# Kernel tuning notes

Measured on AMD Instinct MI355X. Metric: run time of the kernel, lower is better.

The kernel has to match this reference:

```python
import jax, jax.numpy as jnp
import numpy as np

M_DIM = 128   # vec_dim m
L_BAS = 64    # bas_dim L
RANK = 8      # sliding window length
BATCH = 32
SEQ = 2048


def _make_bbasis(L, m):
    # Bbasis[k, i] = cos(2*pi*(k+1)/(i+2)), fixed buffer
    k = jnp.arange(L, dtype=jnp.float32)[:, None]
    i = jnp.arange(m, dtype=jnp.float32)[None, :]
    return jnp.cos(2.0 * jnp.pi * (k + 1.0) / (i + 2.0))


def setup_inputs() -> dict:
    key = jax.random.key(0)
    k1, k2 = jax.random.split(key)
    seq_batch = jax.random.normal(k1, (BATCH, SEQ, M_DIM), dtype=jnp.float32)
    M = jnp.eye(M_DIM, dtype=jnp.float32)                     # nn.init.eye_
    Acoeff = jax.random.uniform(k2, (M_DIM, L_BAS), dtype=jnp.float32,
                                minval=-0.1, maxval=0.1)      # uniform(-0.1, 0.1)
    Bbasis = _make_bbasis(L_BAS, M_DIM)
    return {"seq_batch": seq_batch, "M": M, "Acoeff": Acoeff, "Bbasis": Bbasis}


def reference(seq_batch, M, Acoeff, Bbasis):
    B, S, m = seq_batch.shape
    L = Acoeff.shape[1]
    Nw = S - RANK + 1  # number of sliding windows (linear mode, stride 1)

    # unfold-equivalent: gather contiguous windows [B, Nw, RANK, m]
    idx = jnp.arange(Nw)[:, None] + jnp.arange(RANK)[None, :]
    windows = seq_batch[:, idx, :]
    agg = windows.mean(axis=2)              # rank_op='avg' -> [B, Nw, m]
    agg = jnp.einsum('bwm,nm->bwn', agg, M)  # agg @ M.T (linear map)

    # position-indexed basis target: N(k)[i] = Acoeff[i, k%L] * Bbasis[k%L, i]
    kmod = jnp.arange(Nw) % L
    Nk = Acoeff.T[kmod] * Bbasis[kmod]       # [Nw, m]

    # mean squared deviation over all windows / dims
    D = jnp.mean((agg - Nk[None, :, :]) ** 2)
    return D
```

## Files before the change

kernel.cpp:

```cpp
#include <hip/hip_runtime.h>

#define BATCH   32
#define SEQ     2048
#define MDIM    128
#define LBAS    64
#define NW      2041
#define TW      16
#define NTILE   8
#define APAD    136

typedef __attribute__((ext_vector_type(8))) short  short8;
typedef __attribute__((ext_vector_type(4))) float  float4v;

__device__ __forceinline__ unsigned short f2bf(float f) {
    unsigned int u = __float_as_uint(f);
    return (unsigned short)((u + 0x7FFFu + ((u >> 16) & 1u)) >> 16);
}
__device__ __forceinline__ void store_bf16x4(unsigned short* p, float4v a) {
    unsigned int lo = (unsigned)f2bf(a.x) | ((unsigned)f2bf(a.y) << 16);
    unsigned int hi = (unsigned)f2bf(a.z) | ((unsigned)f2bf(a.w) << 16);
    *reinterpret_cast<unsigned long long*>(p) = ((unsigned long long)hi << 32) | lo;
}

__global__ __launch_bounds__(256)
void ndd_prep(const float* __restrict__ Mmat,
              const float* __restrict__ Acoeff,
              const float* __restrict__ Bbasis,
              unsigned short* __restrict__ Mb,
              float* __restrict__ nkT)
{
    const int gid = blockIdx.x * 256 + threadIdx.x;
    if (gid < 2048) {
        const int n = gid >> 4;
        const int c = gid & 15;
        const float* src = Mmat + n * MDIM + c * 8;
        short8 v;
        #pragma unroll
        for (int j = 0; j < 8; ++j) v[j] = (short)f2bf(src[j]);
        *reinterpret_cast<short8*>(Mb + ((size_t)(c * MDIM + n)) * 8) = v;
    } else if (gid < 2048 + 8192) {
        const int e = gid - 2048;
        const int n = e >> 6;
        const int k = e & 63;
        nkT[e] = Acoeff[e] * Bbasis[k * MDIM + n];
    }
}

__global__ __launch_bounds__(256, 2)
void ndd_main(const float* __restrict__ x,
              const unsigned short* __restrict__ Mb,
              const float* __restrict__ nkT,
              float* __restrict__ partial)
{
    __shared__ __align__(16) float sRaw[3][12 * 256];
    __shared__ __align__(16) unsigned short sA[TW * APAD];
    __shared__ float sred[4];

    const int tid  = threadIdx.x;
    const int lane = tid & 63;
    const int wave = tid >> 6;
    const int b    = blockIdx.x >> 4;
    const int base = (blockIdx.x & 15) * 128;
    const float* xb = x + (size_t)b * SEQ * MDIM;

    const int l15 = lane & 15;
    const int q   = lane >> 4;
    const int nb  = wave * 32;

    short8 bfr[4][2];
    #pragma unroll
    for (int kk = 0; kk < 4; ++kk)
        #pragma unroll
        for (int nj = 0; nj < 2; ++nj)
            bfr[kk][nj] = *reinterpret_cast<const short8*>(
                Mb + ((size_t)((kk * 4 + q) * MDIM + nb + nj * 16 + l15)) * 8);

    float4v nkreg[4][2];
    #pragma unroll
    for (int p = 0; p < 4; ++p)
        #pragma unroll
        for (int nj = 0; nj < 2; ++nj)
            nkreg[p][nj] = *reinterpret_cast<const float4v*>(
                nkT + (size_t)(nb + nj * 16 + l15) * LBAS + p * 16 + q * 4);

    auto issue = [&](int j) {
        const int W0r = base + j * TW;
        #pragma unroll
        for (int i = 0; i < 3; ++i) {
            const int c = wave * 3 + i;
            int r0 = W0r + 2 * c;
            r0 = r0 > 2046 ? 2046 : r0;
            const float* g = xb + (size_t)r0 * MDIM + lane * 4;
            __builtin_amdgcn_global_load_lds(
                (const __attribute__((address_space(1))) void*)g,
                (__attribute__((address_space(3))) void*)&sRaw[j % 3][c * 256],
                16, 0, 0);
        }
    };
    issue(0);
    issue(1);

    float local = 0.f;

    #pragma unroll
    for (int j = 0; j < NTILE; ++j) {
        __builtin_amdgcn_sched_barrier(0);
        if (j == NTILE - 1) __builtin_amdgcn_s_waitcnt(0x0F70);
        else                __builtin_amdgcn_s_waitcnt(0x0F73);
        asm volatile("s_barrier" ::: "memory");
        __builtin_amdgcn_sched_barrier(0);

        {
            const int m4 = tid & 31;
            const int wg = tid >> 5;
            const float4v* R = reinterpret_cast<const float4v*>(&sRaw[j % 3][0]);
            float4v rows[9];
            #pragma unroll
            for (int i = 0; i < 9; ++i) rows[i] = R[(wg * 2 + i) * 32 + m4];
            float4v acc = ((rows[0] + rows[1]) + (rows[2] + rows[3])) +
                          ((rows[4] + rows[5]) + (rows[6] + rows[7]));
            store_bf16x4(&sA[(wg * 2) * APAD + m4 * 4], acc * 0.125f);
            acc += rows[8] - rows[0];
            store_bf16x4(&sA[(wg * 2 + 1) * APAD + m4 * 4], acc * 0.125f);
        }

        __builtin_amdgcn_sched_barrier(0);
        __builtin_amdgcn_s_waitcnt(0xC07F);
        asm volatile("s_barrier" ::: "memory");
        __builtin_amdgcn_sched_barrier(0);

        if (j + 2 < NTILE) issue(j + 2);

        float4v accf[2] = {(float4v){0.f,0.f,0.f,0.f}, (float4v){0.f,0.f,0.f,0.f}};
        #pragma unroll
        for (int kk = 0; kk < 4; ++kk) {
            const short8 af = *reinterpret_cast<const short8*>(
                &sA[l15 * APAD + kk * 32 + q * 8]);
            #pragma unroll
            for (int nj = 0; nj < 2; ++nj)
                accf[nj] = __builtin_amdgcn_mfma_f32_16x16x32_bf16(
                    af, bfr[kk][nj], accf[nj], 0, 0, 0);
        }

        const int p = j & 3;
        #pragma unroll
        for (int nj = 0; nj < 2; ++nj) {
            #pragma unroll
            for (int r = 0; r < 4; ++r) {
                const int w = base + j * TW + q * 4 + r;
                if (w < NW) {
                    const float d = accf[nj][r] - nkreg[p][nj][r];
                    local += d * d;
                }
            }
        }
    }

    #pragma unroll
    for (int off = 32; off > 0; off >>= 1)
        local += __shfl_down(local, off, 64);
    if (lane == 0) sred[wave] = local;
    __syncthreads();
    if (tid == 0)
        partial[blockIdx.x] = (sred[0] + sred[1]) + (sred[2] + sred[3]);
}

__global__ __launch_bounds__(256)
void ndd_reduce(const float* __restrict__ partial, float* __restrict__ out)
{
    __shared__ float sred[4];
    float s = partial[threadIdx.x] + partial[threadIdx.x + 256];
    #pragma unroll
    for (int off = 32; off > 0; off >>= 1) s += __shfl_down(s, off, 64);
    if ((threadIdx.x & 63) == 0) sred[threadIdx.x >> 6] = s;
    __syncthreads();
    if (threadIdx.x == 0)
        out[0] = ((sred[0] + sred[1]) + (sred[2] + sred[3])) * (1.0f / 8359936.0f);
}

extern "C" void kernel_launch(void* const* d_in, const int* in_sizes, int n_in,
                              void* d_out, int out_size, void* d_ws, size_t ws_size,
                              hipStream_t stream) {
    const float* x     = (const float*)d_in[0];
    const float* Mmat  = (const float*)d_in[1];
    const float* Acoef = (const float*)d_in[2];
    const float* Bbas  = (const float*)d_in[3];
    float* out         = (float*)d_out;

    unsigned short* Mb = (unsigned short*)d_ws;
    float* nkTp        = (float*)((char*)d_ws + 32768);
    float* part        = (float*)((char*)d_ws + 65536);

    ndd_prep<<<40, 256, 0, stream>>>(Mmat, Acoef, Bbas, Mb, nkTp);
    ndd_main<<<512, 256, 0, stream>>>(x, Mb, nkTp, part);
    ndd_reduce<<<1, 256, 0, stream>>>(part, out);
}
```

Before: 84.15 us.

## Split main kernel into one tile per block with 4096 blocks

```diff
diff --git a/kernel.cpp b/kernel.cpp
--- a/kernel.cpp
+++ b/kernel.cpp
@@ -6,7 +6,7 @@
 #define LBAS    64
 #define NW      2041
 #define TW      16
-#define NTILE   8
+#define NBLK    4096
 #define APAD    136
 
 typedef __attribute__((ext_vector_type(8))) short  short8;
@@ -46,22 +46,37 @@
     }
 }
 
-__global__ __launch_bounds__(256, 2)
+__global__ __launch_bounds__(256, 4)
 void ndd_main(const float* __restrict__ x,
               const unsigned short* __restrict__ Mb,
               const float* __restrict__ nkT,
               float* __restrict__ partial)
 {
-    __shared__ __align__(16) float sRaw[3][12 * 256];
+    __shared__ __align__(16) float sRaw[12 * 256];
     __shared__ __align__(16) unsigned short sA[TW * APAD];
     __shared__ float sred[4];
 
     const int tid  = threadIdx.x;
     const int lane = tid & 63;
     const int wave = tid >> 6;
-    const int b    = blockIdx.x >> 4;
-    const int base = (blockIdx.x & 15) * 128;
+
+    const int w0   = (blockIdx.x & 7) * (NBLK / 8) + (blockIdx.x >> 3);
+    const int b    = w0 >> 7;
+    const int t    = w0 & 127;
+    const int base = t * TW;
     const float* xb = x + (size_t)b * SEQ * MDIM;
+
+    #pragma unroll
+    for (int i = 0; i < 3; ++i) {
+        const int c = wave * 3 + i;
+        int r0 = base + 2 * c;
+        r0 = r0 > 2046 ? 2046 : r0;
+        const float* g = xb + (size_t)r0 * MDIM + lane * 4;
+        __builtin_amdgcn_global_load_lds(
+            (const __attribute__((address_space(1))) void*)g,
+            (__attribute__((address_space(3))) void*)&sRaw[c * 256],
+            16, 0, 0);
+    }
 
     const int l15 = lane & 15;
     const int q   = lane >> 4;
@@ -75,83 +90,51 @@
             bfr[kk][nj] = *reinterpret_cast<const short8*>(
                 Mb + ((size_t)((kk * 4 + q) * MDIM + nb + nj * 16 + l15)) * 8);
 
-    float4v nkreg[4][2];
+    const int p = t & 3;
+    float4v nkreg[2];
     #pragma unroll
-    for (int p = 0; p < 4; ++p)
+    for (int nj = 0; nj < 2; ++nj)
+        nkreg[nj] = *reinterpret_cast<const float4v*>(
+            nkT + (size_t)(nb + nj * 16 + l15) * LBAS + p * 16 + q * 4);
+
+    __syncthreads();
+
+    {
+        const int m4 = tid & 31;
+        const int wg = tid >> 5;
+        const float4v* R = reinterpret_cast<const float4v*>(&sRaw[0]);
+        float4v rows[9];
+        #pragma unroll
+        for (int i = 0; i < 9; ++i) rows[i] = R[(wg * 2 + i) * 32 + m4];
+        float4v acc = ((rows[0] + rows[1]) + (rows[2] + rows[3])) +
+                      ((rows[4] + rows[5]) + (rows[6] + rows[7]));
+        store_bf16x4(&sA[(wg * 2) * APAD + m4 * 4], acc * 0.125f);
+        acc += rows[8] - rows[0];
+        store_bf16x4(&sA[(wg * 2 + 1) * APAD + m4 * 4], acc * 0.125f);
+    }
+
+    __syncthreads();
+
+    float4v accf[2] = {(float4v){0.f,0.f,0.f,0.f}, (float4v){0.f,0.f,0.f,0.f}};
+    #pragma unroll
+    for (int kk = 0; kk < 4; ++kk) {
+        const short8 af = *reinterpret_cast<const short8*>(
+            &sA[l15 * APAD + kk * 32 + q * 8]);
         #pragma unroll
         for (int nj = 0; nj < 2; ++nj)
-            nkreg[p][nj] = *reinterpret_cast<const float4v*>(
-                nkT + (size_t)(nb + nj * 16 + l15) * LBAS + p * 16 + q * 4);
-
-    auto issue = [&](int j) {
-        const int W0r = base + j * TW;
-        #pragma unroll
-        for (int i = 0; i < 3; ++i) {
-            const int c = wave * 3 + i;
-            int r0 = W0r + 2 * c;
-            r0 = r0 > 2046 ? 2046 : r0;
-            const float* g = xb + (size_t)r0 * MDIM + lane * 4;
-            __builtin_amdgcn_global_load_lds(
-                (const __attribute__((address_space(1))) void*)g,
-                (__attribute__((address_space(3))) void*)&sRaw[j % 3][c * 256],
-                16, 0, 0);
-        }
-    };
-    issue(0);
-    issue(1);
+            accf[nj] = __builtin_amdgcn_mfma_f32_16x16x32_bf16(
+                af, bfr[kk][nj], accf[nj], 0, 0, 0);
+    }
 
     float local = 0.f;
-
     #pragma unroll
-    for (int j = 0; j < NTILE; ++j) {
-        __builtin_amdgcn_sched_barrier(0);
-        if (j == NTILE - 1) __builtin_amdgcn_s_waitcnt(0x0F70);
-        else                __builtin_amdgcn_s_waitcnt(0x0F73);
-        asm volatile("s_barrier" ::: "memory");
-        __builtin_amdgcn_sched_barrier(0);
-
-        {
-            const int m4 = tid & 31;
-            const int wg = tid >> 5;
-            const float4v* R = reinterpret_cast<const float4v*>(&sRaw[j % 3][0]);
-            float4v rows[9];
-            #pragma unroll
-            for (int i = 0; i < 9; ++i) rows[i] = R[(wg * 2 + i) * 32 + m4];
-            float4v acc = ((rows[0] + rows[1]) + (rows[2] + rows[3])) +
-                          ((rows[4] + rows[5]) + (rows[6] + rows[7]));
-            store_bf16x4(&sA[(wg * 2) * APAD + m4 * 4], acc * 0.125f);
-            acc += rows[8] - rows[0];
-            store_bf16x4(&sA[(wg * 2 + 1) * APAD + m4 * 4], acc * 0.125f);
-        }
-
-        __builtin_amdgcn_sched_barrier(0);
-        __builtin_amdgcn_s_waitcnt(0xC07F);
-        asm volatile("s_barrier" ::: "memory");
-        __builtin_amdgcn_sched_barrier(0);
-
-        if (j + 2 < NTILE) issue(j + 2);
-
-        float4v accf[2] = {(float4v){0.f,0.f,0.f,0.f}, (float4v){0.f,0.f,0.f,0.f}};
+    for (int nj = 0; nj < 2; ++nj) {
         #pragma unroll
-        for (int kk = 0; kk < 4; ++kk) {
-            const short8 af = *reinterpret_cast<const short8*>(
-                &sA[l15 * APAD + kk * 32 + q * 8]);
-            #pragma unroll
-            for (int nj = 0; nj < 2; ++nj)
-                accf[nj] = __builtin_amdgcn_mfma_f32_16x16x32_bf16(
-                    af, bfr[kk][nj], accf[nj], 0, 0, 0);
-        }
-
-        const int p = j & 3;
-        #pragma unroll
-        for (int nj = 0; nj < 2; ++nj) {
-            #pragma unroll
-            for (int r = 0; r < 4; ++r) {
-                const int w = base + j * TW + q * 4 + r;
-                if (w < NW) {
-                    const float d = accf[nj][r] - nkreg[p][nj][r];
-                    local += d * d;
-                }
+        for (int r = 0; r < 4; ++r) {
+            const int w = base + q * 4 + r;
+            if (w < NW) {
+                const float d = accf[nj][r] - nkreg[nj][r];
+                local += d * d;
             }
         }
     }
@@ -169,7 +152,10 @@
 void ndd_reduce(const float* __restrict__ partial, float* __restrict__ out)
 {
     __shared__ float sred[4];
-    float s = partial[threadIdx.x] + partial[threadIdx.x + 256];
+    float s = 0.f;
+    #pragma unroll
+    for (int i = 0; i < NBLK / 256; ++i)
+        s += partial[threadIdx.x + i * 256];
     #pragma unroll
     for (int off = 32; off > 0; off >>= 1) s += __shfl_down(s, off, 64);
     if ((threadIdx.x & 63) == 0) sred[threadIdx.x >> 6] = s;
@@ -192,6 +178,6 @@
     float* part        = (float*)((char*)d_ws + 65536);
 
     ndd_prep<<<40, 256, 0, stream>>>(Mmat, Acoef, Bbas, Mb, nkTp);
-    ndd_main<<<512, 256, 0, stream>>>(x, Mb, nkTp, part);
+    ndd_main<<<NBLK, 256, 0, stream>>>(x, Mb, nkTp, part);
     ndd_reduce<<<1, 256, 0, stream>>>(part, out);
 }
```

New measurement: 90.54 us. 7.6% more time.

## Replace LDS pipelined tile loads with direct register loads and per-wave sliding sums

Applied to the files above, without the earlier changes.

```diff
diff --git a/kernel.cpp b/kernel.cpp
--- a/kernel.cpp
+++ b/kernel.cpp
@@ -5,21 +5,16 @@
 #define MDIM    128
 #define LBAS    64
 #define NW      2041
-#define TW      16
-#define NTILE   8
 #define APAD    136
+#define NBLK    512
 
 typedef __attribute__((ext_vector_type(8))) short  short8;
 typedef __attribute__((ext_vector_type(4))) float  float4v;
+typedef __attribute__((ext_vector_type(2))) float  float2v;
 
 __device__ __forceinline__ unsigned short f2bf(float f) {
     unsigned int u = __float_as_uint(f);
     return (unsigned short)((u + 0x7FFFu + ((u >> 16) & 1u)) >> 16);
-}
-__device__ __forceinline__ void store_bf16x4(unsigned short* p, float4v a) {
-    unsigned int lo = (unsigned)f2bf(a.x) | ((unsigned)f2bf(a.y) << 16);
-    unsigned int hi = (unsigned)f2bf(a.z) | ((unsigned)f2bf(a.w) << 16);
-    *reinterpret_cast<unsigned long long*>(p) = ((unsigned long long)hi << 32) | lo;
 }
 
 __global__ __launch_bounds__(256)
@@ -52,8 +47,7 @@
               const float* __restrict__ nkT,
               float* __restrict__ partial)
 {
-    __shared__ __align__(16) float sRaw[3][12 * 256];
-    __shared__ __align__(16) unsigned short sA[TW * APAD];
+    __shared__ __align__(16) unsigned short sA[128 * APAD];
     __shared__ float sred[4];
 
     const int tid  = threadIdx.x;
@@ -63,10 +57,19 @@
     const int base = (blockIdx.x & 15) * 128;
     const float* xb = x + (size_t)b * SEQ * MDIM;
 
+    const int r0 = base + wave * 32;
+    float2v rows[39];
+    #pragma unroll
+    for (int k = 0; k < 39; ++k) {
+        int rr = r0 + k;
+        rr = rr > 2047 ? 2047 : rr;
+        rows[k] = *reinterpret_cast<const float2v*>(
+            xb + (size_t)rr * MDIM + lane * 2);
+    }
+
     const int l15 = lane & 15;
     const int q   = lane >> 4;
     const int nb  = wave * 32;
-
     short8 bfr[4][2];
     #pragma unroll
     for (int kk = 0; kk < 4; ++kk)
@@ -74,7 +77,6 @@
         for (int nj = 0; nj < 2; ++nj)
             bfr[kk][nj] = *reinterpret_cast<const short8*>(
                 Mb + ((size_t)((kk * 4 + q) * MDIM + nb + nj * 16 + l15)) * 8);
-
     float4v nkreg[4][2];
     #pragma unroll
     for (int p = 0; p < 4; ++p)
@@ -83,71 +85,43 @@
             nkreg[p][nj] = *reinterpret_cast<const float4v*>(
                 nkT + (size_t)(nb + nj * 16 + l15) * LBAS + p * 16 + q * 4);
 
-    auto issue = [&](int j) {
-        const int W0r = base + j * TW;
-        #pragma unroll
-        for (int i = 0; i < 3; ++i) {
-            const int c = wave * 3 + i;
-            int r0 = W0r + 2 * c;
-            r0 = r0 > 2046 ? 2046 : r0;
-            const float* g = xb + (size_t)r0 * MDIM + lane * 4;
-            __builtin_amdgcn_global_load_lds(
-                (const __attribute__((address_space(1))) void*)g,
-                (__attribute__((address_space(3))) void*)&sRaw[j % 3][c * 256],
-                16, 0, 0);
-        }
-    };
-    issue(0);
-    issue(1);
+    unsigned short* myA = sA + (size_t)(wave * 32) * APAD + lane * 2;
+    float2v s = ((rows[0] + rows[1]) + (rows[2] + rows[3])) +
+                ((rows[4] + rows[5]) + (rows[6] + rows[7]));
+    {
+        float2v m = s * 0.125f;
+        *reinterpret_cast<unsigned int*>(myA) =
+            (unsigned)f2bf(m.x) | ((unsigned)f2bf(m.y) << 16);
+    }
+    #pragma unroll
+    for (int w = 1; w < 32; ++w) {
+        s += rows[w + 7] - rows[w - 1];
+        float2v m = s * 0.125f;
+        *reinterpret_cast<unsigned int*>(myA + (size_t)w * APAD) =
+            (unsigned)f2bf(m.x) | ((unsigned)f2bf(m.y) << 16);
+    }
+
+    __syncthreads();
 
     float local = 0.f;
-
     #pragma unroll
-    for (int j = 0; j < NTILE; ++j) {
-        __builtin_amdgcn_sched_barrier(0);
-        if (j == NTILE - 1) __builtin_amdgcn_s_waitcnt(0x0F70);
-        else                __builtin_amdgcn_s_waitcnt(0x0F73);
-        asm volatile("s_barrier" ::: "memory");
-        __builtin_amdgcn_sched_barrier(0);
-
-        {
-            const int m4 = tid & 31;
-            const int wg = tid >> 5;
-            const float4v* R = reinterpret_cast<const float4v*>(&sRaw[j % 3][0]);
-            float4v rows[9];
-            #pragma unroll
-            for (int i = 0; i < 9; ++i) rows[i] = R[(wg * 2 + i) * 32 + m4];
-            float4v acc = ((rows[0] + rows[1]) + (rows[2] + rows[3])) +
-                          ((rows[4] + rows[5]) + (rows[6] + rows[7]));
-            store_bf16x4(&sA[(wg * 2) * APAD + m4 * 4], acc * 0.125f);
-            acc += rows[8] - rows[0];
-            store_bf16x4(&sA[(wg * 2 + 1) * APAD + m4 * 4], acc * 0.125f);
-        }
-
-        __builtin_amdgcn_sched_barrier(0);
-        __builtin_amdgcn_s_waitcnt(0xC07F);
-        asm volatile("s_barrier" ::: "memory");
-        __builtin_amdgcn_sched_barrier(0);
-
-        if (j + 2 < NTILE) issue(j + 2);
-
+    for (int wg = 0; wg < 8; ++wg) {
         float4v accf[2] = {(float4v){0.f,0.f,0.f,0.f}, (float4v){0.f,0.f,0.f,0.f}};
         #pragma unroll
         for (int kk = 0; kk < 4; ++kk) {
             const short8 af = *reinterpret_cast<const short8*>(
-                &sA[l15 * APAD + kk * 32 + q * 8]);
+                &sA[(wg * 16 + l15) * APAD + kk * 32 + q * 8]);
             #pragma unroll
             for (int nj = 0; nj < 2; ++nj)
                 accf[nj] = __builtin_amdgcn_mfma_f32_16x16x32_bf16(
                     af, bfr[kk][nj], accf[nj], 0, 0, 0);
         }
-
-        const int p = j & 3;
+        const int p = wg & 3;
         #pragma unroll
         for (int nj = 0; nj < 2; ++nj) {
             #pragma unroll
             for (int r = 0; r < 4; ++r) {
-                const int w = base + j * TW + q * 4 + r;
+                const int w = base + wg * 16 + q * 4 + r;
                 if (w < NW) {
                     const float d = accf[nj][r] - nkreg[p][nj][r];
                     local += d * d;
@@ -192,6 +166,6 @@
     float* part        = (float*)((char*)d_ws + 65536);
 
     ndd_prep<<<40, 256, 0, stream>>>(Mmat, Acoef, Bbas, Mb, nkTp);
-    ndd_main<<<512, 256, 0, stream>>>(x, Mb, nkTp, part);
+    ndd_main<<<NBLK, 256, 0, stream>>>(x, Mb, nkTp, part);
     ndd_reduce<<<1, 256, 0, stream>>>(part, out);
 }
```

Measured after the change: 83.96 us. About the same (-0.2%).
